# Kernel tuning notes

Measured on AMD Instinct MI355X. Metric: run time of the kernel, lower is better.

The kernel has to match this reference:

```python
import jax, jax.numpy as jnp
import numpy as np

B, H, P, L = 8, 512, 512, 2048
HIGH_STAB, LOW_STAB = 0.9, 0.99  # 0 <= high < |lambda| <= low <= 1 (discrete dynamics)


def setup_inputs() -> dict:
    key = jax.random.key(0)
    k_u, k_mag, k_ph, k_b, k_c, k_d = jax.random.split(key, 6)
    u = jax.random.normal(k_u, (B, H, L), dtype=jnp.float32)
    # Frozen diagonal reservoir state matrix Lambda_bar: complex eigenvalues with
    # magnitude in (high_stability, low_stability], random phase (stored as real/imag pairs).
    mag = jax.random.uniform(k_mag, (P,), minval=HIGH_STAB, maxval=LOW_STAB)
    phase = jax.random.uniform(k_ph, (P,), minval=0.0, maxval=2.0 * np.pi)
    Lambda_bar_ri = jnp.stack([mag * jnp.cos(phase), mag * jnp.sin(phase)], axis=-1)  # (P,2)
    B_bar_ri = jax.random.normal(k_b, (P, H, 2), dtype=jnp.float32)  # complex B_bar as real pairs
    C_ri = jax.random.normal(k_c, (H, P, 2), dtype=jnp.float32)      # complex C as real pairs
    D = jax.random.normal(k_d, (H, H), dtype=jnp.float32)
    return {"u": u, "Lambda_bar_ri": Lambda_bar_ri, "B_bar_ri": B_bar_ri, "C_ri": C_ri, "D": D}


def _binary_op(e_i, e_j):
    A_i, Bu_i = e_i
    A_j, Bu_j = e_j
    return (A_j * A_i, A_j * Bu_i + Bu_j)


def reference(u, Lambda_bar_ri, B_bar_ri, C_ri, D):
    Lam = jax.lax.complex(Lambda_bar_ri[:, 0], Lambda_bar_ri[:, 1])        # (P,)
    B_bar = jax.lax.complex(B_bar_ri[..., 0], B_bar_ri[..., 1])            # (P,H)
    C = jax.lax.complex(C_ri[..., 0], C_ri[..., 1])                        # (H,P)
    # Bu_t = B_bar @ u_t for all t, batched: (B,P,L) complex
    Bu = jnp.einsum('ph,bhl->bpl', B_bar, u.astype(B_bar.dtype))
    A = jnp.broadcast_to(Lam[None, :, None], Bu.shape)                     # (B,P,L)
    # Parallel associative scan: x_t = Lam * x_{t-1} + Bu_t
    _, x = jax.lax.associative_scan(_binary_op, (A, Bu), axis=2)           # (B,P,L)
    C_A_Bu = jnp.einsum('hp,bpl->bhl', C, x).real                          # (B,H,L)
    # torch.einsum('hh,bhl->bhl', D, u) uses only the diagonal of D
    Du = jnp.diagonal(D)[None, :, None] * u
    return jax.nn.gelu(C_A_Bu + Du, approximate=False)
```

## Files before the change

kernel.cpp:

```cpp
#include <hip/hip_runtime.h>
#include <cstdint>
#include <cstddef>

#define BB 8
#define HH 512
#define PP 512
#define LL 2048

typedef __attribute__((ext_vector_type(8))) __bf16 bf16x8;
typedef __attribute__((ext_vector_type(4))) float f32x4;

__device__ __forceinline__ uint16_t f2bf(float f) {
  uint32_t u = __builtin_bit_cast(uint32_t, f);
  u += 0x7FFFu + ((u >> 16) & 1u);
  return (uint16_t)(u >> 16);
}

__device__ __forceinline__ void async_copy16(const void* gptr, void* ldsptr) {
  __builtin_amdgcn_global_load_lds(
      (const __attribute__((address_space(1))) unsigned int*)gptr,
      (__attribute__((address_space(3))) unsigned int*)ldsptr,
      16, 0, 0);
}

__global__ __launch_bounds__(256) void prep_and_transpose(
    const float* __restrict__ U, const float* __restrict__ Bbar,
    const float* __restrict__ Cri, const float* __restrict__ Dm,
    uint16_t* __restrict__ Ut, uint16_t* __restrict__ A1,
    uint16_t* __restrict__ A2, float* __restrict__ Dd) {
  __shared__ uint16_t tile[64][66];
  const int t = threadIdx.x;
  if (blockIdx.x < 2048) {
    const int bid = blockIdx.x;
    const int b = bid >> 8;
    const int h0 = ((bid >> 5) & 7) * 64;
    const int l0 = (bid & 31) * 64;
    const int r = t >> 2, c = t & 3;
    const float* src = U + ((size_t)(b * 512 + h0 + r)) * 2048 + l0 + c * 16;
#pragma unroll
    for (int q = 0; q < 4; ++q) {
      float4 v = *(const float4*)(src + q * 4);
      *(uint32_t*)&tile[r][c * 16 + q * 4]     = (uint32_t)f2bf(v.x) | ((uint32_t)f2bf(v.y) << 16);
      *(uint32_t*)&tile[r][c * 16 + q * 4 + 2] = (uint32_t)f2bf(v.z) | ((uint32_t)f2bf(v.w) << 16);
    }
    __syncthreads();
    uint16_t* dst = Ut + ((size_t)(b * 2048 + l0 + r)) * 512 + h0 + c * 16;
    uint32_t o[8];
#pragma unroll
    for (int k = 0; k < 8; ++k)
      o[k] = (uint32_t)tile[c * 16 + 2 * k][r] | ((uint32_t)tile[c * 16 + 2 * k + 1][r] << 16);
    *(uint4*)(dst)     = make_uint4(o[0], o[1], o[2], o[3]);
    *(uint4*)(dst + 8) = make_uint4(o[4], o[5], o[6], o[7]);
  } else {
    int idx = (blockIdx.x - 2048) * 256 + t;
    int p = idx >> 9, h = idx & 511;
    A1[(size_t)p * 512 + h]          = f2bf(Bbar[((size_t)p * 512 + h) * 2 + 0]);
    A1[(size_t)(512 + p) * 512 + h]  = f2bf(Bbar[((size_t)p * 512 + h) * 2 + 1]);
    int h2 = idx >> 9, p2 = idx & 511;
    A2[(size_t)h2 * 1024 + p2]        = f2bf( Cri[((size_t)h2 * 512 + p2) * 2 + 0]);
    A2[(size_t)h2 * 1024 + 512 + p2]  = f2bf(-Cri[((size_t)h2 * 512 + p2) * 2 + 1]);
    if (idx < 512) Dd[idx] = Dm[(size_t)idx * 512 + idx];
  }
}

__global__ __launch_bounds__(256) void scan_kernel(
    const float* __restrict__ Lam, uint16_t* __restrict__ Bu) {
  const int gt = blockIdx.x * 256 + threadIdx.x;
  const int wave = gt >> 6, lane = gt & 63;
  const int b = wave >> 9, p = wave & 511;
  const float lr = Lam[p * 2 + 0], li = Lam[p * 2 + 1];
  float ar = lr, ai = li;
#pragma unroll
  for (int s = 0; s < 5; ++s) { float nr = ar * ar - ai * ai, ni = 2.f * ar * ai; ar = nr; ai = ni; }

  uint16_t* rowre = Bu + ((size_t)(b * 1024 + p)) * 2048 + lane * 32;
  uint16_t* rowim = Bu + ((size_t)(b * 1024 + 512 + p)) * 2048 + lane * 32;
  uint4 vr[4], vi[4];
#pragma unroll
  for (int q = 0; q < 4; ++q) { vr[q] = ((const uint4*)rowre)[q]; vi[q] = ((const uint4*)rowim)[q]; }

  float xr[32], xi[32];
  float sr = 0.f, si = 0.f;
#pragma unroll
  for (int q = 0; q < 4; ++q) {
    uint32_t wr[4] = {vr[q].x, vr[q].y, vr[q].z, vr[q].w};
    uint32_t wi[4] = {vi[q].x, vi[q].y, vi[q].z, vi[q].w};
#pragma unroll
    for (int d = 0; d < 4; ++d) {
      float br0 = __builtin_bit_cast(float, wr[d] << 16);
      float bi0 = __builtin_bit_cast(float, wi[d] << 16);
      float br1 = __builtin_bit_cast(float, wr[d] & 0xFFFF0000u);
      float bi1 = __builtin_bit_cast(float, wi[d] & 0xFFFF0000u);
      int j = q * 8 + d * 2;
      float nr = lr * sr - li * si + br0, ni = lr * si + li * sr + bi0;
      sr = nr; si = ni; xr[j] = sr; xi[j] = si;
      nr = lr * sr - li * si + br1; ni = lr * si + li * sr + bi1;
      sr = nr; si = ni; xr[j + 1] = sr; xi[j + 1] = si;
    }
  }
  float Ar = ar, Ai = ai, Sr = sr, Si = si;
#pragma unroll
  for (int off = 1; off < 64; off <<= 1) {
    float pAr = __shfl_up(Ar, off), pAi = __shfl_up(Ai, off);
    float pSr = __shfl_up(Sr, off), pSi = __shfl_up(Si, off);
    if (lane >= off) {
      float tSr = Ar * pSr - Ai * pSi + Sr;
      float tSi = Ar * pSi + Ai * pSr + Si;
      float tAr = Ar * pAr - Ai * pAi;
      float tAi = Ar * pAi + Ai * pAr;
      Sr = tSr; Si = tSi; Ar = tAr; Ai = tAi;
    }
  }
  float Cr = __shfl_up(Sr, 1), Ci = __shfl_up(Si, 1);
  if (lane == 0) { Cr = 0.f; Ci = 0.f; }
  float fr_ = lr * Cr - li * Ci, fi_ = lr * Ci + li * Cr;
#pragma unroll
  for (int j = 0; j < 32; ++j) {
    xr[j] += fr_; xi[j] += fi_;
    float nfr = fr_ * lr - fi_ * li, nfi = fr_ * li + fi_ * lr;
    fr_ = nfr; fi_ = nfi;
  }
#pragma unroll
  for (int q = 0; q < 4; ++q) {
    uint32_t wr[4], wi[4];
#pragma unroll
    for (int d = 0; d < 4; ++d) {
      int j = q * 8 + d * 2;
      wr[d] = (uint32_t)f2bf(xr[j]) | ((uint32_t)f2bf(xr[j + 1]) << 16);
      wi[d] = (uint32_t)f2bf(xi[j]) | ((uint32_t)f2bf(xi[j + 1]) << 16);
    }
    ((uint4*)rowre)[q] = make_uint4(wr[0], wr[1], wr[2], wr[3]);
    ((uint4*)rowim)[q] = make_uint4(wi[0], wi[1], wi[2], wi[3]);
  }
}

__global__ __launch_bounds__(256) void transpose_x(
    const uint16_t* __restrict__ X, uint16_t* __restrict__ Xt) {
  __shared__ uint16_t tile[64][66];
  const int t = threadIdx.x;
  const int b = blockIdx.z, p0 = blockIdx.y * 64, l0 = blockIdx.x * 64;
  const int r = t >> 2, c = t & 3;
  const uint16_t* src = X + ((size_t)(b * 1024 + p0 + r)) * 2048 + l0 + c * 16;
  uint4 v0 = *(const uint4*)(src);
  uint4 v1 = *(const uint4*)(src + 8);
  *(uint32_t*)&tile[r][c * 16 + 0]  = v0.x;
  *(uint32_t*)&tile[r][c * 16 + 2]  = v0.y;
  *(uint32_t*)&tile[r][c * 16 + 4]  = v0.z;
  *(uint32_t*)&tile[r][c * 16 + 6]  = v0.w;
  *(uint32_t*)&tile[r][c * 16 + 8]  = v1.x;
  *(uint32_t*)&tile[r][c * 16 + 10] = v1.y;
  *(uint32_t*)&tile[r][c * 16 + 12] = v1.z;
  *(uint32_t*)&tile[r][c * 16 + 14] = v1.w;
  __syncthreads();
  uint16_t* dst = Xt + ((size_t)(b * 2048 + l0 + r)) * 1024 + p0 + c * 16;
  uint32_t o[8];
#pragma unroll
  for (int k = 0; k < 8; ++k)
    o[k] = (uint32_t)tile[c * 16 + 2 * k][r] | ((uint32_t)tile[c * 16 + 2 * k + 1][r] << 16);
  *(uint4*)(dst)     = make_uint4(o[0], o[1], o[2], o[3]);
  *(uint4*)(dst + 8) = make_uint4(o[4], o[5], o[6], o[7]);
}

#define GEMM_CORE(KDIM)                                                       \
  constexpr int K = (KDIM), NT = K / 32;                                      \
  __shared__ __align__(16) uint16_t Alds[3][128 * 32];                        \
  __shared__ __align__(16) uint16_t Blds[3][64 * 32];                         \
  const int t = threadIdx.x, lane = t & 63, w = t >> 6;                       \
  const int m0 = blockIdx.y * 128, n0 = blockIdx.x * 64, b = blockIdx.z;      \
  const int r0 = t >> 2;                                                      \
  const int c0 = (t & 3) ^ ((r0 >> 1) & 3);                                   \
  const uint16_t* pA0 = Amat + (size_t)(m0 + r0) * K + c0 * 8;                \
  const uint16_t* pA1 = Amat + (size_t)(m0 + 64 + r0) * K + c0 * 8;           \
  const uint16_t* pB0 = Bt + ((size_t)b * 2048 + n0 + r0) * K + c0 * 8;       \
  const int d0 = t * 8;                                                       \
  const int wm = (w >> 1) * 64, wn = (w & 1) * 32;                            \
  const int fr = lane & 15, fq = lane >> 4;                                   \
  int offA[4], offB[2];                                                       \
  _Pragma("unroll")                                                           \
  for (int i = 0; i < 4; ++i) {                                               \
    int rm = wm + i * 16 + fr;                                                \
    offA[i] = rm * 32 + ((fq ^ ((rm >> 1) & 3)) * 8);                         \
  }                                                                           \
  _Pragma("unroll")                                                           \
  for (int j = 0; j < 2; ++j) {                                               \
    int rn = wn + j * 16 + fr;                                                \
    offB[j] = rn * 32 + ((fq ^ ((rn >> 1) & 3)) * 8);                         \
  }                                                                           \
  f32x4 acc[4][2];                                                            \
  _Pragma("unroll")                                                           \
  for (int i = 0; i < 4; ++i)                                                 \
    _Pragma("unroll")                                                         \
    for (int j = 0; j < 2; ++j) acc[i][j] = (f32x4){0.f, 0.f, 0.f, 0.f};      \
            \
  async_copy16(pA0,      &Alds[0][d0]);                                       \
  async_copy16(pA1,      &Alds[0][2048 + d0]);                                \
  async_copy16(pB0,      &Blds[0][d0]);                                       \
  async_copy16(pA0 + 32, &Alds[1][d0]);                                       \
  async_copy16(pA1 + 32, &Alds[1][2048 + d0]);                                \
  async_copy16(pB0 + 32, &Blds[1][d0]);                                       \
  _Pragma("unroll")                                                           \
  for (int kt = 0; kt < NT; ++kt) {                                           \
    const int cur = kt % 3;                                                   \
    if (kt + 1 < NT) asm volatile("s_waitcnt vmcnt(3)" ::: "memory");         \
    else             asm volatile("s_waitcnt vmcnt(0)" ::: "memory");         \
    __builtin_amdgcn_s_barrier();                                             \
    __builtin_amdgcn_sched_barrier(0);                                        \
    if (kt + 2 < NT) {                                                        \
      const int nb = (kt + 2) % 3;                                            \
      const int kb = (kt + 2) * 32;                                           \
      async_copy16(pA0 + kb, &Alds[nb][d0]);                                  \
      async_copy16(pA1 + kb, &Alds[nb][2048 + d0]);                           \
      async_copy16(pB0 + kb, &Blds[nb][d0]);                                  \
    }                                                                         \
    bf16x8 af[4], bv[2];                                                      \
    _Pragma("unroll")                                                         \
    for (int i = 0; i < 4; ++i) af[i] = *(const bf16x8*)&Alds[cur][offA[i]];  \
    _Pragma("unroll")                                                         \
    for (int j = 0; j < 2; ++j) bv[j] = *(const bf16x8*)&Blds[cur][offB[j]];  \
    _Pragma("unroll")                                                         \
    for (int i = 0; i < 4; ++i)                                               \
      _Pragma("unroll")                                                       \
      for (int j = 0; j < 2; ++j)                                             \
        acc[i][j] = __builtin_amdgcn_mfma_f32_16x16x32_bf16(af[i], bv[j], acc[i][j], 0, 0, 0); \
  }

__global__ __launch_bounds__(256) void gemm1_fused(
    const uint16_t* __restrict__ Amat, const uint16_t* __restrict__ Bt,
    uint16_t* __restrict__ Bu) {
  GEMM_CORE(512)
  uint16_t* O = Bu + ((size_t)b * 1024 + m0) * 2048 + n0;
#pragma unroll
  for (int i = 0; i < 4; ++i)
#pragma unroll
    for (int j = 0; j < 2; ++j)
#pragma unroll
      for (int r = 0; r < 4; ++r) {
        int mm = wm + i * 16 + fq * 4 + r;
        int nn = wn + j * 16 + fr;
        O[(size_t)mm * 2048 + nn] = f2bf(acc[i][j][r]);
      }
}

__global__ __launch_bounds__(256) void gemm2_fused(
    const uint16_t* __restrict__ Amat, const uint16_t* __restrict__ Bt,
    float* __restrict__ Out, const float* __restrict__ Dd,
    const float* __restrict__ Uu) {
  GEMM_CORE(1024)
  const size_t base = ((size_t)b * 512 + m0) * 2048 + n0;
  float* O = Out + base;
  const float* Ub = Uu + base;
#pragma unroll
  for (int i = 0; i < 4; ++i)
#pragma unroll
    for (int r = 0; r < 4; ++r) {
      int mm = wm + i * 16 + fq * 4 + r;
      float dv = Dd[m0 + mm];
#pragma unroll
      for (int j = 0; j < 2; ++j) {
        int nn = wn + j * 16 + fr;
        float xv = acc[i][j][r] + dv * Ub[(size_t)mm * 2048 + nn];
        O[(size_t)mm * 2048 + nn] = 0.5f * xv * (1.f + erff(xv * 0.70710678118654752f));
      }
    }
}

extern "C" void kernel_launch(void* const* d_in, const int* in_sizes, int n_in,
                              void* d_out, int out_size, void* d_ws, size_t ws_size,
                              hipStream_t stream) {
  const float* u    = (const float*)d_in[0];
  const float* Lam  = (const float*)d_in[1];
  const float* Bbar = (const float*)d_in[2];
  const float* Cri  = (const float*)d_in[3];
  const float* Dm   = (const float*)d_in[4];
  float* out = (float*)d_out;

  char* ws = (char*)d_ws;
  uint16_t* Bu = (uint16_t*)(ws);
  uint16_t* Xt = (uint16_t*)(ws + 33554432);
  uint16_t* Ut = (uint16_t*)(ws + 33554432);
  uint16_t* A1 = (uint16_t*)(ws + 67108864);
  uint16_t* A2 = (uint16_t*)(ws + 68157440);
  float*    Dd = (float*)   (ws + 69206016);

  prep_and_transpose<<<3072, 256, 0, stream>>>(u, Bbar, Cri, Dm, Ut, A1, A2, Dd);
  gemm1_fused<<<dim3(32, 8, BB), 256, 0, stream>>>(A1, Ut, Bu);
  scan_kernel<<<1024, 256, 0, stream>>>(Lam, Bu);
  transpose_x<<<dim3(32, 16, BB), 256, 0, stream>>>(Bu, Xt);
  gemm2_fused<<<dim3(32, 4, BB), 256, 0, stream>>>(A2, Xt, out, Dd, u);
}
```

Baseline: 187.7 us.

## Fuse scan with transpose into blocked-K layout consumed directly by gemm2

Replaces the separate scan kernel (which wrote its result back to Bu in place) and the transpose kernel with one kernel. It runs the complex scan for 8 state rows per block, stages the bf16 results in shared memory, and writes them in a k-blocked layout of 8-element groups per time step. gemm2's B-operand addressing is adjusted to read that layout with a per-k-tile stride. This removes one launch and a full read/write pass of the 32 MB intermediate. The cost is 64 KB of LDS per 512-thread block, which lowers occupancy of the scan, plus 2-byte strided LDS reads during the transpose.

```diff
diff --git a/kernel.cpp b/kernel.cpp
--- a/kernel.cpp
+++ b/kernel.cpp
@@ -63,18 +63,20 @@
   }
 }
 
-__global__ __launch_bounds__(256) void scan_kernel(
-    const float* __restrict__ Lam, uint16_t* __restrict__ Bu) {
-  const int gt = blockIdx.x * 256 + threadIdx.x;
-  const int wave = gt >> 6, lane = gt & 63;
-  const int b = wave >> 9, p = wave & 511;
+__global__ __launch_bounds__(512) void scan_tr(
+    const float* __restrict__ Lam, const uint16_t* __restrict__ Bu,
+    uint16_t* __restrict__ Xt8) {
+  __shared__ uint16_t S[16][2048];
+  const int t = threadIdx.x, wave = t >> 6, lane = t & 63;
+  const int b = blockIdx.x >> 6, p0 = (blockIdx.x & 63) * 8, p = p0 + wave;
+
   const float lr = Lam[p * 2 + 0], li = Lam[p * 2 + 1];
   float ar = lr, ai = li;
 #pragma unroll
   for (int s = 0; s < 5; ++s) { float nr = ar * ar - ai * ai, ni = 2.f * ar * ai; ar = nr; ai = ni; }
 
-  uint16_t* rowre = Bu + ((size_t)(b * 1024 + p)) * 2048 + lane * 32;
-  uint16_t* rowim = Bu + ((size_t)(b * 1024 + 512 + p)) * 2048 + lane * 32;
+  const uint16_t* rowre = Bu + ((size_t)(b * 1024 + p)) * 2048 + lane * 32;
+  const uint16_t* rowim = Bu + ((size_t)(b * 1024 + 512 + p)) * 2048 + lane * 32;
   uint4 vr[4], vi[4];
 #pragma unroll
   for (int q = 0; q < 4; ++q) { vr[q] = ((const uint4*)rowre)[q]; vi[q] = ((const uint4*)rowim)[q]; }
@@ -129,39 +131,27 @@
       wr[d] = (uint32_t)f2bf(xr[j]) | ((uint32_t)f2bf(xr[j + 1]) << 16);
       wi[d] = (uint32_t)f2bf(xi[j]) | ((uint32_t)f2bf(xi[j + 1]) << 16);
     }
-    ((uint4*)rowre)[q] = make_uint4(wr[0], wr[1], wr[2], wr[3]);
-    ((uint4*)rowim)[q] = make_uint4(wi[0], wi[1], wi[2], wi[3]);
-  }
-}
-
-__global__ __launch_bounds__(256) void transpose_x(
-    const uint16_t* __restrict__ X, uint16_t* __restrict__ Xt) {
-  __shared__ uint16_t tile[64][66];
-  const int t = threadIdx.x;
-  const int b = blockIdx.z, p0 = blockIdx.y * 64, l0 = blockIdx.x * 64;
-  const int r = t >> 2, c = t & 3;
-  const uint16_t* src = X + ((size_t)(b * 1024 + p0 + r)) * 2048 + l0 + c * 16;
-  uint4 v0 = *(const uint4*)(src);
-  uint4 v1 = *(const uint4*)(src + 8);
-  *(uint32_t*)&tile[r][c * 16 + 0]  = v0.x;
-  *(uint32_t*)&tile[r][c * 16 + 2]  = v0.y;
-  *(uint32_t*)&tile[r][c * 16 + 4]  = v0.z;
-  *(uint32_t*)&tile[r][c * 16 + 6]  = v0.w;
-  *(uint32_t*)&tile[r][c * 16 + 8]  = v1.x;
-  *(uint32_t*)&tile[r][c * 16 + 10] = v1.y;
-  *(uint32_t*)&tile[r][c * 16 + 12] = v1.z;
-  *(uint32_t*)&tile[r][c * 16 + 14] = v1.w;
+    *(uint4*)&S[wave * 2 + 0][lane * 32 + q * 8] = make_uint4(wr[0], wr[1], wr[2], wr[3]);
+    *(uint4*)&S[wave * 2 + 1][lane * 32 + q * 8] = make_uint4(wi[0], wi[1], wi[2], wi[3]);
+  }
   __syncthreads();
-  uint16_t* dst = Xt + ((size_t)(b * 2048 + l0 + r)) * 1024 + p0 + c * 16;
-  uint32_t o[8];
-#pragma unroll
-  for (int k = 0; k < 8; ++k)
-    o[k] = (uint32_t)tile[c * 16 + 2 * k][r] | ((uint32_t)tile[c * 16 + 2 * k + 1][r] << 16);
-  *(uint4*)(dst)     = make_uint4(o[0], o[1], o[2], o[3]);
-  *(uint4*)(dst + 8) = make_uint4(o[4], o[5], o[6], o[7]);
-}
-
-#define GEMM_CORE(KDIM)                                                       \
+  const size_t gre = (size_t)b * 128 + (p0 >> 3);
+#pragma unroll
+  for (int c = 0; c < 2; ++c) {
+    uint16_t* dst = Xt8 + (gre + (size_t)c * 64) * 2048 * 8;
+#pragma unroll
+    for (int rep = 0; rep < 4; ++rep) {
+      int l = rep * 512 + t;
+      uint32_t o0 = (uint32_t)S[0 + c][l] | ((uint32_t)S[2 + c][l] << 16);
+      uint32_t o1 = (uint32_t)S[4 + c][l] | ((uint32_t)S[6 + c][l] << 16);
+      uint32_t o2 = (uint32_t)S[8 + c][l] | ((uint32_t)S[10 + c][l] << 16);
+      uint32_t o3 = (uint32_t)S[12 + c][l] | ((uint32_t)S[14 + c][l] << 16);
+      *(uint4*)(dst + (size_t)l * 8) = make_uint4(o0, o1, o2, o3);
+    }
+  }
+}
+
+#define GEMM_CORE(KDIM, PB0_EXPR, BSTRIDE)                                    \
   constexpr int K = (KDIM), NT = K / 32;                                      \
   __shared__ __align__(16) uint16_t Alds[3][128 * 32];                        \
   __shared__ __align__(16) uint16_t Blds[3][64 * 32];                         \
@@ -171,7 +161,7 @@
   const int c0 = (t & 3) ^ ((r0 >> 1) & 3);                                   \
   const uint16_t* pA0 = Amat + (size_t)(m0 + r0) * K + c0 * 8;                \
   const uint16_t* pA1 = Amat + (size_t)(m0 + 64 + r0) * K + c0 * 8;           \
-  const uint16_t* pB0 = Bt + ((size_t)b * 2048 + n0 + r0) * K + c0 * 8;       \
+  const uint16_t* pB0 = (PB0_EXPR);                                           \
   const int d0 = t * 8;                                                       \
   const int wm = (w >> 1) * 64, wn = (w & 1) * 32;                            \
   const int fr = lane & 15, fq = lane >> 4;                                   \
@@ -192,12 +182,12 @@
     _Pragma("unroll")                                                         \
     for (int j = 0; j < 2; ++j) acc[i][j] = (f32x4){0.f, 0.f, 0.f, 0.f};      \
             \
-  async_copy16(pA0,      &Alds[0][d0]);                                       \
-  async_copy16(pA1,      &Alds[0][2048 + d0]);                                \
-  async_copy16(pB0,      &Blds[0][d0]);                                       \
-  async_copy16(pA0 + 32, &Alds[1][d0]);                                       \
-  async_copy16(pA1 + 32, &Alds[1][2048 + d0]);                                \
-  async_copy16(pB0 + 32, &Blds[1][d0]);                                       \
+  async_copy16(pA0,             &Alds[0][d0]);                                \
+  async_copy16(pA1,             &Alds[0][2048 + d0]);                         \
+  async_copy16(pB0,             &Blds[0][d0]);                                \
+  async_copy16(pA0 + 32,        &Alds[1][d0]);                                \
+  async_copy16(pA1 + 32,        &Alds[1][2048 + d0]);                         \
+  async_copy16(pB0 + (BSTRIDE), &Blds[1][d0]);                                \
   _Pragma("unroll")                                                           \
   for (int kt = 0; kt < NT; ++kt) {                                           \
     const int cur = kt % 3;                                                   \
@@ -210,7 +200,7 @@
       const int kb = (kt + 2) * 32;                                           \
       async_copy16(pA0 + kb, &Alds[nb][d0]);                                  \
       async_copy16(pA1 + kb, &Alds[nb][2048 + d0]);                           \
-      async_copy16(pB0 + kb, &Blds[nb][d0]);                                  \
+      async_copy16(pB0 + (size_t)(kt + 2) * (BSTRIDE), &Blds[nb][d0]);        \
     }                                                                         \
     bf16x8 af[4], bv[2];                                                      \
     _Pragma("unroll")                                                         \
@@ -227,7 +217,7 @@
 __global__ __launch_bounds__(256) void gemm1_fused(
     const uint16_t* __restrict__ Amat, const uint16_t* __restrict__ Bt,
     uint16_t* __restrict__ Bu) {
-  GEMM_CORE(512)
+  GEMM_CORE(512, Bt + ((size_t)b * 2048 + n0 + r0) * 512 + c0 * 8, 32)
   uint16_t* O = Bu + ((size_t)b * 1024 + m0) * 2048 + n0;
 #pragma unroll
   for (int i = 0; i < 4; ++i)
@@ -245,7 +235,7 @@
     const uint16_t* __restrict__ Amat, const uint16_t* __restrict__ Bt,
     float* __restrict__ Out, const float* __restrict__ Dd,
     const float* __restrict__ Uu) {
-  GEMM_CORE(1024)
+  GEMM_CORE(1024, Bt + (((size_t)b * 128 + c0) * 2048 + n0 + r0) * 8, 65536)
   const size_t base = ((size_t)b * 512 + m0) * 2048 + n0;
   float* O = Out + base;
   const float* Ub = Uu + base;
@@ -275,16 +265,15 @@
   float* out = (float*)d_out;
 
   char* ws = (char*)d_ws;
-  uint16_t* Bu = (uint16_t*)(ws);
-  uint16_t* Xt = (uint16_t*)(ws + 33554432);
-  uint16_t* Ut = (uint16_t*)(ws + 33554432);
+  uint16_t* Bu  = (uint16_t*)(ws);
+  uint16_t* Xt8 = (uint16_t*)(ws + 33554432);
+  uint16_t* Ut  = (uint16_t*)(ws + 33554432);
   uint16_t* A1 = (uint16_t*)(ws + 67108864);
   uint16_t* A2 = (uint16_t*)(ws + 68157440);
   float*    Dd = (float*)   (ws + 69206016);
 
   prep_and_transpose<<<3072, 256, 0, stream>>>(u, Bbar, Cri, Dm, Ut, A1, A2, Dd);
   gemm1_fused<<<dim3(32, 8, BB), 256, 0, stream>>>(A1, Ut, Bu);
-  scan_kernel<<<1024, 256, 0, stream>>>(Lam, Bu);
-  transpose_x<<<dim3(32, 16, BB), 256, 0, stream>>>(Bu, Xt);
-  gemm2_fused<<<dim3(32, 4, BB), 256, 0, stream>>>(A2, Xt, out, Dd, u);
-}
+  scan_tr<<<512, 512, 0, stream>>>(Lam, Bu, Xt8);
+  gemm2_fused<<<dim3(32, 4, BB), 256, 0, stream>>>(A2, Xt8, out, Dd, u);
+}
```

Result: faster. 172.8 us (-7.9%).
